# Kernel tuning notes

Measured on AMD Instinct MI355X. Metric: run time of the kernel, lower is better.

The kernel has to match this reference:

```python
import jax, jax.numpy as jnp
import numpy as np

EPS = 1e-6

def setup_inputs() -> dict:
    key = jax.random.key(0)
    ks = jax.random.split(key, 4)
    T, B, D = 2048, 16, 1024
    x = jax.random.normal(ks[0], (T, B, D), dtype=jnp.float32)
    h0 = jax.random.normal(ks[1], (B, D), dtype=jnp.float32)
    # xavier_uniform bound for square [D, D] matrices
    bound = float(np.sqrt(6.0 / (D + D)))
    W = jax.random.uniform(ks[2], (D, D), dtype=jnp.float32, minval=-bound, maxval=bound)
    W_g = jax.random.uniform(ks[3], (D, D), dtype=jnp.float32, minval=-bound, maxval=bound)
    b = jnp.zeros((D,), dtype=jnp.float32)
    b_g = jnp.full((D,), -2.0, dtype=jnp.float32)
    return {"x": x, "h0": h0, "W": W, "W_g": W_g, "b": b, "b_g": b_g}

def reference(x, h0, W, W_g, b, b_g):
    # Precompute both projections in batch (as the torch module does)
    Wx_all = jnp.einsum('tbd,ed->tbe', x, W) + b            # [T, B, D]
    gate_all = jax.nn.sigmoid(jnp.einsum('tbd,ed->tbe', x, W_g) + b_g)

    def step(h, inp):
        g, wx = inp
        h_new = h + g * wx                                   # gated residual
        h_new = h_new * jax.lax.rsqrt(
            jnp.mean(h_new * h_new, axis=-1, keepdims=True) + EPS)  # RMSNorm
        out = h_new * jax.nn.silu(h_new)                     # h * silu(h)
        return h_new, (h_new, out)

    _, (hs, outs) = jax.lax.scan(step, h0, (gate_all, Wx_all))
    h = jnp.concatenate([h0[None], hs], axis=0)              # [T+1, B, D]
    return outs, h
```

## Files before the change

kernel.cpp:

```cpp
#include <hip/hip_runtime.h>
#include <hip/hip_fp16.h>

typedef _Float16 f16;
typedef _Float16 f16x8 __attribute__((ext_vector_type(8)));
typedef float    f32x2 __attribute__((ext_vector_type(2)));
typedef float    f32x4 __attribute__((ext_vector_type(4)));
typedef unsigned ui4   __attribute__((ext_vector_type(4)));

#define T_STEPS 2048
#define BATCH   16
#define DIM     1024

__device__ __forceinline__ void async16(void* lds, const void* g) {
  __builtin_amdgcn_global_load_lds(
      (const __attribute__((address_space(1))) void*)g,
      (__attribute__((address_space(3))) void*)lds, 16, 0, 0);
}

__device__ __forceinline__ float fma_mix_lo(unsigned p, float one, float h) {
  float d;
  asm("v_fma_mix_f32 %0, %1, %2, %3 op_sel:[0,0,0] op_sel_hi:[1,0,0]"
      : "=v"(d) : "v"(p), "v"(one), "v"(h));
  return d;
}
__device__ __forceinline__ float fma_mix_hi(unsigned p, float one, float h) {
  float d;
  asm("v_fma_mix_f32 %0, %1, %2, %3 op_sel:[1,0,0] op_sel_hi:[1,0,0]"
      : "=v"(d) : "v"(p), "v"(one), "v"(h));
  return d;
}

__global__ void cvt_kernel(const float* __restrict__ src, f16* __restrict__ dst,
                           int n8) {
  int i = blockIdx.x * 256 + threadIdx.x;
  if (i >= n8) return;
  const float4* s4 = reinterpret_cast<const float4*>(src);
  float4 a = s4[2 * i], b = s4[2 * i + 1];
  f16x8 o;
  o[0] = (f16)a.x; o[1] = (f16)a.y; o[2] = (f16)a.z; o[3] = (f16)a.w;
  o[4] = (f16)b.x; o[5] = (f16)b.y; o[6] = (f16)b.z; o[7] = (f16)b.w;
  *reinterpret_cast<f16x8*>(dst + (size_t)i * 8) = o;
}

__global__ __launch_bounds__(256, 2)
void dual_gemm(const f16* __restrict__ xh, const f16* __restrict__ wh,
               const f16* __restrict__ wgh, const float* __restrict__ bias,
               const float* __restrict__ biasg, f16* __restrict__ P) {
  __shared__ f16 As[128 * 32];
  __shared__ f16 Bs[128 * 32];
  __shared__ f16 Gs[128 * 32];

  const int tid = threadIdx.x;
  const int bid = blockIdx.x;
  const int swz = ((bid & 7) << 8) | (bid >> 3);
  const int m0 = (swz >> 3) * 128;
  const int e0 = (swz & 7) * 128;

  const int lane = tid & 63;
  const int wave = tid >> 6;
  const int wrow = (wave >> 1) * 64;
  const int wcol = (wave & 1) * 64;
  const int fr = lane & 15;
  const int fc = lane >> 4;

  f32x4 acc1[4][4], acc2[4][4];
#pragma unroll
  for (int i = 0; i < 4; ++i)
#pragma unroll
    for (int j = 0; j < 4; ++j) {
      acc1[i][j] = {0.f, 0.f, 0.f, 0.f};
      acc2[i][j] = {0.f, 0.f, 0.f, 0.f};
    }

  const int    srow  = tid >> 2;
  const size_t sbyte = (size_t)(tid & 3) * 16;
  const char* ga = (const char*)xh  + ((size_t)(m0 + srow)) * 2048 + sbyte;
  const char* gb = (const char*)wh  + ((size_t)(e0 + srow)) * 2048 + sbyte;
  const char* gg = (const char*)wgh + ((size_t)(e0 + srow)) * 2048 + sbyte;
  char* la = (char*)&As[0] + (size_t)wave * 1024;
  char* lb = (char*)&Bs[0] + (size_t)wave * 1024;
  char* lg = (char*)&Gs[0] + (size_t)wave * 1024;

  for (int kk = 0; kk < 1024; kk += 32) {
    const size_t ko = (size_t)kk * 2;
    async16(la,        ga + ko);
    async16(la + 4096, ga + ko + (size_t)64 * 2048);
    async16(lb,        gb + ko);
    async16(lb + 4096, gb + ko + (size_t)64 * 2048);
    async16(lg,        gg + ko);
    async16(lg + 4096, gg + ko + (size_t)64 * 2048);
    asm volatile("s_waitcnt vmcnt(0)" ::: "memory");
    __syncthreads();

    f16x8 af[4], bf[4], gf[4];
#pragma unroll
    for (int i = 0; i < 4; ++i) {
      af[i] = *reinterpret_cast<const f16x8*>(&As[(wrow + i * 16 + fr) * 32 + fc * 8]);
      bf[i] = *reinterpret_cast<const f16x8*>(&Bs[(wcol + i * 16 + fr) * 32 + fc * 8]);
      gf[i] = *reinterpret_cast<const f16x8*>(&Gs[(wcol + i * 16 + fr) * 32 + fc * 8]);
    }
#pragma unroll
    for (int mi = 0; mi < 4; ++mi)
#pragma unroll
      for (int ni = 0; ni < 4; ++ni) {
        acc1[mi][ni] = __builtin_amdgcn_mfma_f32_16x16x32_f16(af[mi], bf[ni], acc1[mi][ni], 0, 0, 0);
        acc2[mi][ni] = __builtin_amdgcn_mfma_f32_16x16x32_f16(af[mi], gf[ni], acc2[mi][ni], 0, 0, 0);
      }
    __syncthreads();
  }

#pragma unroll
  for (int ni = 0; ni < 4; ++ni) {
    const int e = e0 + wcol + ni * 16 + fr;
    const float bb  = bias[e];
    const float bbg = biasg[e];
#pragma unroll
    for (int mi = 0; mi < 4; ++mi) {
      const int mrow = m0 + wrow + mi * 16 + fc * 4;
#pragma unroll
      for (int j = 0; j < 4; ++j) {
        float z1 = acc1[mi][ni][j] + bb;
        float z2 = acc2[mi][ni][j] + bbg;
        float s  = 1.0f / (1.0f + __expf(-z2));
        P[(size_t)(mrow + j) * DIM + e] = (f16)(z1 * s);
      }
    }
  }
}

template <int CTRL>
__device__ __forceinline__ float dpp_add(float x) {
  int m = __builtin_amdgcn_update_dpp(0, __float_as_int(x), CTRL, 0xf, 0xf, true);
  return x + __int_as_float(m);
}

__global__ __launch_bounds__(64, 1)
void scan_kernel(const f16* __restrict__ P, const float* __restrict__ h0,
                 float* __restrict__ hout) {
  const int b = blockIdx.x;
  const int lane = threadIdx.x;

  f32x4 h4[4];
  {
    const f32x4* s = (const f32x4*)(h0 + (size_t)b * DIM);
    f32x4* d = (f32x4*)(hout + (size_t)b * DIM);
    h4[0] = s[2 * lane];       d[2 * lane]       = h4[0];
    h4[1] = s[2 * lane + 1];   d[2 * lane + 1]   = h4[1];
    h4[2] = s[128 + 2 * lane]; d[128 + 2 * lane] = h4[2];
    h4[3] = s[129 + 2 * lane]; d[129 + 2 * lane] = h4[3];
  }

  ui4 pf[8][2];
#pragma unroll
  for (int u = 0; u < 8; ++u) {
    const ui4* pr = (const ui4*)(P + ((size_t)u * BATCH + b) * DIM);
    pf[u][0] = pr[lane];
    pf[u][1] = pr[64 + lane];
  }

  const float one = 1.0f;

  for (int t0 = 0; t0 < T_STEPS; t0 += 8) {
#pragma unroll
    for (int u = 0; u < 8; ++u) {
      const int t = t0 + u;

      f32x4 v4[4];
#pragma unroll
      for (int c = 0; c < 4; ++c) {
        const unsigned w0 = pf[u][c >> 1][(c & 1) * 2];
        const unsigned w1 = pf[u][c >> 1][(c & 1) * 2 + 1];
        v4[c][0] = fma_mix_lo(w0, one, h4[c][0]);
        v4[c][1] = fma_mix_hi(w0, one, h4[c][1]);
        v4[c][2] = fma_mix_lo(w1, one, h4[c][2]);
        v4[c][3] = fma_mix_hi(w1, one, h4[c][3]);
      }

      {
        const int tp = (t + 8) & (T_STEPS - 1);
        const ui4* pr = (const ui4*)(P + ((size_t)tp * BATCH + b) * DIM);
        pf[u][0] = pr[lane];
        pf[u][1] = pr[64 + lane];
      }

      f32x2 sE, sO;
      {
        f32x2 e0v = __builtin_shufflevector(v4[0], v4[0], 0, 1);
        f32x2 o0v = __builtin_shufflevector(v4[0], v4[0], 2, 3);
        sE = e0v * e0v;
        sO = o0v * o0v;
#pragma unroll
        for (int c = 1; c < 4; ++c) {
          f32x2 ec = __builtin_shufflevector(v4[c], v4[c], 0, 1);
          f32x2 oc = __builtin_shufflevector(v4[c], v4[c], 2, 3);
          sE += ec * ec;
          sO += oc * oc;
        }
      }
      f32x2 sC = sE + sO;
      float ss = sC[0] + sC[1];
      ss = dpp_add<0x111>(ss);
      ss = dpp_add<0x112>(ss);
      ss = dpp_add<0x114>(ss);
      ss = dpp_add<0x118>(ss);
      ss = dpp_add<0x142>(ss);
      ss = dpp_add<0x143>(ss);
      float tot = __int_as_float(__builtin_amdgcn_readlane(__float_as_int(ss), 63));
      float r = __builtin_amdgcn_rsqf(fmaf(tot, 9.765625e-4f, 1e-6f));

#pragma unroll
      for (int c = 0; c < 4; ++c) h4[c] = v4[c] * r;

      f32x4* hr = (f32x4*)(hout + ((size_t)(t + 1) * BATCH + b) * DIM);
      hr[2 * lane]       = h4[0];
      hr[2 * lane + 1]   = h4[1];
      hr[128 + 2 * lane] = h4[2];
      hr[129 + 2 * lane] = h4[3];
    }
  }
}

__global__ void silu_out_kernel(const float* __restrict__ hsrc,
                                float* __restrict__ out, int n4) {
  int stride = gridDim.x * blockDim.x;
  for (int i = blockIdx.x * blockDim.x + threadIdx.x; i < n4; i += stride) {
    float4 v = reinterpret_cast<const float4*>(hsrc)[i];
    float4 o;
    o.x = v.x * v.x / (1.0f + __expf(-v.x));
    o.y = v.y * v.y / (1.0f + __expf(-v.y));
    o.z = v.z * v.z / (1.0f + __expf(-v.z));
    o.w = v.w * v.w / (1.0f + __expf(-v.w));
    reinterpret_cast<float4*>(out)[i] = o;
  }
}

extern "C" void kernel_launch(void* const* d_in, const int* in_sizes, int n_in,
                              void* d_out, int out_size, void* d_ws, size_t ws_size,
                              hipStream_t stream) {
  const float* x  = (const float*)d_in[0];
  const float* h0 = (const float*)d_in[1];
  const float* W  = (const float*)d_in[2];
  const float* Wg = (const float*)d_in[3];
  const float* bb = (const float*)d_in[4];
  const float* bg = (const float*)d_in[5];

  float* out  = (float*)d_out;
  float* hout = out + (size_t)T_STEPS * BATCH * DIM;

  char* ws = (char*)d_ws;
  f16* xh  = (f16*)(ws);
  f16* wh  = (f16*)(ws + (size_t)67108864);
  f16* wgh = (f16*)(ws + (size_t)69206016);
  f16* P   = (f16*)(ws + (size_t)71303168);

  cvt_kernel<<<16384, 256, 0, stream>>>(x,  xh,  4194304);
  cvt_kernel<<<512,   256, 0, stream>>>(W,  wh,  131072);
  cvt_kernel<<<512,   256, 0, stream>>>(Wg, wgh, 131072);

  dual_gemm<<<2048, 256, 0, stream>>>(xh, wh, wgh, bb, bg, P);

  scan_kernel<<<BATCH, 64, 0, stream>>>(P, h0, hout);

  silu_out_kernel<<<2048, 256, 0, stream>>>(hout + BATCH * DIM, out, 8388608);
}
```

Measured before the change: 549.6 us.

## Fuse GEMM and scan into one persistent kernel with per-band readiness counters

Merges the dual GEMM and the sequential scan into one launch. The first 16 blocks run the scan and spin on per-band atomic counters, while the remaining blocks compute GEMM tiles in time order and signal completion with a release atomic. The aim is to overlap the long serial scan with GEMM production instead of running them back to back. This drops the block swizzle, which may hurt L2 reuse of the weights. Progress depends on scan blocks not starving GEMM blocks of occupancy, and the spin guard lets a wait give up after a bounded number of tries.

```diff
diff --git a/kernel.cpp b/kernel.cpp
--- a/kernel.cpp
+++ b/kernel.cpp
@@ -10,6 +10,9 @@
 #define T_STEPS 2048
 #define BATCH   16
 #define DIM     1024
+#define NBANDS  256
+#define SCAN_BLOCKS 16
+#define GEMM_BLOCKS 2048
 
 __device__ __forceinline__ void async16(void* lds, const void* g) {
   __builtin_amdgcn_global_load_lds(
@@ -28,6 +31,16 @@
   asm("v_fma_mix_f32 %0, %1, %2, %3 op_sel:[1,0,0] op_sel_hi:[1,0,0]"
       : "=v"(d) : "v"(p), "v"(one), "v"(h));
   return d;
+}
+
+template <int CTRL>
+__device__ __forceinline__ float dpp_add(float x) {
+  int m = __builtin_amdgcn_update_dpp(0, __float_as_int(x), CTRL, 0xf, 0xf, true);
+  return x + __int_as_float(m);
+}
+
+__global__ void init_kernel(unsigned* __restrict__ cnt) {
+  cnt[threadIdx.x + blockIdx.x * 256] = 0u;
 }
 
 __global__ void cvt_kernel(const float* __restrict__ src, f16* __restrict__ dst,
@@ -43,18 +56,124 @@
 }
 
 __global__ __launch_bounds__(256, 2)
-void dual_gemm(const f16* __restrict__ xh, const f16* __restrict__ wh,
-               const f16* __restrict__ wgh, const float* __restrict__ bias,
-               const float* __restrict__ biasg, f16* __restrict__ P) {
+void mega_kernel(const f16* __restrict__ xh, const f16* __restrict__ wh,
+                 const f16* __restrict__ wgh, const float* __restrict__ bias,
+                 const float* __restrict__ biasg, f16* __restrict__ P,
+                 const float* __restrict__ h0, float* __restrict__ hout,
+                 unsigned* __restrict__ cnt) {
   __shared__ f16 As[128 * 32];
   __shared__ f16 Bs[128 * 32];
   __shared__ f16 Gs[128 * 32];
 
+  if (blockIdx.x < SCAN_BLOCKS) {
+    if (threadIdx.x >= 64) return;
+    const int b = blockIdx.x;
+    const int lane = threadIdx.x;
+
+    {
+      int guard = 1 << 27;
+      while (__hip_atomic_load(&cnt[0], __ATOMIC_RELAXED,
+                               __HIP_MEMORY_SCOPE_AGENT) < 8u && --guard)
+        __builtin_amdgcn_s_sleep(2);
+      (void)__hip_atomic_load(&cnt[0], __ATOMIC_ACQUIRE,
+                              __HIP_MEMORY_SCOPE_AGENT);
+    }
+
+    f32x4 h4[4];
+    {
+      const f32x4* s = (const f32x4*)(h0 + (size_t)b * DIM);
+      f32x4* d = (f32x4*)(hout + (size_t)b * DIM);
+      h4[0] = s[2 * lane];       d[2 * lane]       = h4[0];
+      h4[1] = s[2 * lane + 1];   d[2 * lane + 1]   = h4[1];
+      h4[2] = s[128 + 2 * lane]; d[128 + 2 * lane] = h4[2];
+      h4[3] = s[129 + 2 * lane]; d[129 + 2 * lane] = h4[3];
+    }
+
+    ui4 pf[8][2];
+#pragma unroll
+    for (int u = 0; u < 8; ++u) {
+      const ui4* pr = (const ui4*)(P + ((size_t)u * BATCH + b) * DIM);
+      pf[u][0] = pr[lane];
+      pf[u][1] = pr[64 + lane];
+    }
+
+    const float one = 1.0f;
+
+    for (int t0 = 0; t0 < T_STEPS; t0 += 8) {
+      const int nb = (t0 >> 3) + 1;
+      if (nb < NBANDS) {
+        int guard = 1 << 27;
+        while (__hip_atomic_load(&cnt[nb], __ATOMIC_RELAXED,
+                                 __HIP_MEMORY_SCOPE_AGENT) < 8u && --guard)
+          __builtin_amdgcn_s_sleep(2);
+        (void)__hip_atomic_load(&cnt[nb], __ATOMIC_ACQUIRE,
+                                __HIP_MEMORY_SCOPE_AGENT);
+      }
+#pragma unroll
+      for (int u = 0; u < 8; ++u) {
+        const int t = t0 + u;
+
+        f32x4 v4[4];
+#pragma unroll
+        for (int c = 0; c < 4; ++c) {
+          const unsigned w0 = pf[u][c >> 1][(c & 1) * 2];
+          const unsigned w1 = pf[u][c >> 1][(c & 1) * 2 + 1];
+          v4[c][0] = fma_mix_lo(w0, one, h4[c][0]);
+          v4[c][1] = fma_mix_hi(w0, one, h4[c][1]);
+          v4[c][2] = fma_mix_lo(w1, one, h4[c][2]);
+          v4[c][3] = fma_mix_hi(w1, one, h4[c][3]);
+        }
+
+        {
+          const int tp = (t + 8) & (T_STEPS - 1);
+          const ui4* pr = (const ui4*)(P + ((size_t)tp * BATCH + b) * DIM);
+          pf[u][0] = pr[lane];
+          pf[u][1] = pr[64 + lane];
+        }
+
+        f32x2 sE, sO;
+        {
+          f32x2 e0v = __builtin_shufflevector(v4[0], v4[0], 0, 1);
+          f32x2 o0v = __builtin_shufflevector(v4[0], v4[0], 2, 3);
+          sE = e0v * e0v;
+          sO = o0v * o0v;
+#pragma unroll
+          for (int c = 1; c < 4; ++c) {
+            f32x2 ec = __builtin_shufflevector(v4[c], v4[c], 0, 1);
+            f32x2 oc = __builtin_shufflevector(v4[c], v4[c], 2, 3);
+            sE += ec * ec;
+            sO += oc * oc;
+          }
+        }
+        f32x2 sC = sE + sO;
+        float ss = sC[0] + sC[1];
+        ss = dpp_add<0x111>(ss);
+        ss = dpp_add<0x112>(ss);
+        ss = dpp_add<0x114>(ss);
+        ss = dpp_add<0x118>(ss);
+        ss = dpp_add<0x142>(ss);
+        ss = dpp_add<0x143>(ss);
+        float tot = __int_as_float(__builtin_amdgcn_readlane(__float_as_int(ss), 63));
+        float r = __builtin_amdgcn_rsqf(fmaf(tot, 9.765625e-4f, 1e-6f));
+
+#pragma unroll
+        for (int c = 0; c < 4; ++c) h4[c] = v4[c] * r;
+
+        f32x4* hr = (f32x4*)(hout + ((size_t)(t + 1) * BATCH + b) * DIM);
+        hr[2 * lane]       = h4[0];
+        hr[2 * lane + 1]   = h4[1];
+        hr[128 + 2 * lane] = h4[2];
+        hr[129 + 2 * lane] = h4[3];
+      }
+    }
+    return;
+  }
+
+  const int g = blockIdx.x - SCAN_BLOCKS;
+  const int band = g >> 3;
+  const int m0 = band << 7;
+  const int e0 = (g & 7) << 7;
   const int tid = threadIdx.x;
-  const int bid = blockIdx.x;
-  const int swz = ((bid & 7) << 8) | (bid >> 3);
-  const int m0 = (swz >> 3) * 128;
-  const int e0 = (swz & 7) * 128;
 
   const int lane = tid & 63;
   const int wave = tid >> 6;
@@ -126,98 +245,12 @@
       }
     }
   }
-}
-
-template <int CTRL>
-__device__ __forceinline__ float dpp_add(float x) {
-  int m = __builtin_amdgcn_update_dpp(0, __float_as_int(x), CTRL, 0xf, 0xf, true);
-  return x + __int_as_float(m);
-}
-
-__global__ __launch_bounds__(64, 1)
-void scan_kernel(const f16* __restrict__ P, const float* __restrict__ h0,
-                 float* __restrict__ hout) {
-  const int b = blockIdx.x;
-  const int lane = threadIdx.x;
-
-  f32x4 h4[4];
-  {
-    const f32x4* s = (const f32x4*)(h0 + (size_t)b * DIM);
-    f32x4* d = (f32x4*)(hout + (size_t)b * DIM);
-    h4[0] = s[2 * lane];       d[2 * lane]       = h4[0];
-    h4[1] = s[2 * lane + 1];   d[2 * lane + 1]   = h4[1];
-    h4[2] = s[128 + 2 * lane]; d[128 + 2 * lane] = h4[2];
-    h4[3] = s[129 + 2 * lane]; d[129 + 2 * lane] = h4[3];
-  }
-
-  ui4 pf[8][2];
-#pragma unroll
-  for (int u = 0; u < 8; ++u) {
-    const ui4* pr = (const ui4*)(P + ((size_t)u * BATCH + b) * DIM);
-    pf[u][0] = pr[lane];
-    pf[u][1] = pr[64 + lane];
-  }
-
-  const float one = 1.0f;
-
-  for (int t0 = 0; t0 < T_STEPS; t0 += 8) {
-#pragma unroll
-    for (int u = 0; u < 8; ++u) {
-      const int t = t0 + u;
-
-      f32x4 v4[4];
-#pragma unroll
-      for (int c = 0; c < 4; ++c) {
-        const unsigned w0 = pf[u][c >> 1][(c & 1) * 2];
-        const unsigned w1 = pf[u][c >> 1][(c & 1) * 2 + 1];
-        v4[c][0] = fma_mix_lo(w0, one, h4[c][0]);
-        v4[c][1] = fma_mix_hi(w0, one, h4[c][1]);
-        v4[c][2] = fma_mix_lo(w1, one, h4[c][2]);
-        v4[c][3] = fma_mix_hi(w1, one, h4[c][3]);
-      }
-
-      {
-        const int tp = (t + 8) & (T_STEPS - 1);
-        const ui4* pr = (const ui4*)(P + ((size_t)tp * BATCH + b) * DIM);
-        pf[u][0] = pr[lane];
-        pf[u][1] = pr[64 + lane];
-      }
-
-      f32x2 sE, sO;
-      {
-        f32x2 e0v = __builtin_shufflevector(v4[0], v4[0], 0, 1);
-        f32x2 o0v = __builtin_shufflevector(v4[0], v4[0], 2, 3);
-        sE = e0v * e0v;
-        sO = o0v * o0v;
-#pragma unroll
-        for (int c = 1; c < 4; ++c) {
-          f32x2 ec = __builtin_shufflevector(v4[c], v4[c], 0, 1);
-          f32x2 oc = __builtin_shufflevector(v4[c], v4[c], 2, 3);
-          sE += ec * ec;
-          sO += oc * oc;
-        }
-      }
-      f32x2 sC = sE + sO;
-      float ss = sC[0] + sC[1];
-      ss = dpp_add<0x111>(ss);
-      ss = dpp_add<0x112>(ss);
-      ss = dpp_add<0x114>(ss);
-      ss = dpp_add<0x118>(ss);
-      ss = dpp_add<0x142>(ss);
-      ss = dpp_add<0x143>(ss);
-      float tot = __int_as_float(__builtin_amdgcn_readlane(__float_as_int(ss), 63));
-      float r = __builtin_amdgcn_rsqf(fmaf(tot, 9.765625e-4f, 1e-6f));
-
-#pragma unroll
-      for (int c = 0; c < 4; ++c) h4[c] = v4[c] * r;
-
-      f32x4* hr = (f32x4*)(hout + ((size_t)(t + 1) * BATCH + b) * DIM);
-      hr[2 * lane]       = h4[0];
-      hr[2 * lane + 1]   = h4[1];
-      hr[128 + 2 * lane] = h4[2];
-      hr[129 + 2 * lane] = h4[3];
-    }
-  }
+
+  __threadfence();
+  __syncthreads();
+  if (tid == 0)
+    __hip_atomic_fetch_add(&cnt[band], 1u, __ATOMIC_RELEASE,
+                           __HIP_MEMORY_SCOPE_AGENT);
 }
 
 __global__ void silu_out_kernel(const float* __restrict__ hsrc,
@@ -252,14 +285,16 @@
   f16* wh  = (f16*)(ws + (size_t)67108864);
   f16* wgh = (f16*)(ws + (size_t)69206016);
   f16* P   = (f16*)(ws + (size_t)71303168);
+  unsigned* cnt = (unsigned*)(ws + (size_t)138412032);
+
+  init_kernel<<<4, 256, 0, stream>>>(cnt);
 
   cvt_kernel<<<16384, 256, 0, stream>>>(x,  xh,  4194304);
   cvt_kernel<<<512,   256, 0, stream>>>(W,  wh,  131072);
   cvt_kernel<<<512,   256, 0, stream>>>(Wg, wgh, 131072);
 
-  dual_gemm<<<2048, 256, 0, stream>>>(xh, wh, wgh, bb, bg, P);
-
-  scan_kernel<<<BATCH, 64, 0, stream>>>(P, h0, hout);
+  mega_kernel<<<SCAN_BLOCKS + GEMM_BLOCKS, 256, 0, stream>>>(
+      xh, wh, wgh, bb, bg, P, h0, hout, cnt);
 
   silu_out_kernel<<<2048, 256, 0, stream>>>(hout + BATCH * DIM, out, 8388608);
 }
```

After: 969.8 us. 1.76x slower.

## Process two batch rows per wavefront in scan kernel to interleave reductions

Applied to the files above, without the earlier changes.

The scan kernel now assigns two batch rows to each 64-lane block and launches 8 blocks instead of 16. The two rows' fma-mix updates, DPP reduction chains and rsqrt steps are interleaved so each row's serial latency chain can hide the other's. The cost is double the register use (prefetch buffers doubled to 2x8x2 ui4) and only 8 CUs active, so per-wave memory bandwidth for loads and stores doubles.

```diff
diff --git a/kernel.cpp b/kernel.cpp
--- a/kernel.cpp
+++ b/kernel.cpp
@@ -137,26 +137,29 @@
 __global__ __launch_bounds__(64, 1)
 void scan_kernel(const f16* __restrict__ P, const float* __restrict__ h0,
                  float* __restrict__ hout) {
-  const int b = blockIdx.x;
+  const int b0 = blockIdx.x * 2;
   const int lane = threadIdx.x;
 
-  f32x4 h4[4];
-  {
-    const f32x4* s = (const f32x4*)(h0 + (size_t)b * DIM);
-    f32x4* d = (f32x4*)(hout + (size_t)b * DIM);
-    h4[0] = s[2 * lane];       d[2 * lane]       = h4[0];
-    h4[1] = s[2 * lane + 1];   d[2 * lane + 1]   = h4[1];
-    h4[2] = s[128 + 2 * lane]; d[128 + 2 * lane] = h4[2];
-    h4[3] = s[129 + 2 * lane]; d[129 + 2 * lane] = h4[3];
-  }
-
-  ui4 pf[8][2];
-#pragma unroll
-  for (int u = 0; u < 8; ++u) {
-    const ui4* pr = (const ui4*)(P + ((size_t)u * BATCH + b) * DIM);
-    pf[u][0] = pr[lane];
-    pf[u][1] = pr[64 + lane];
-  }
+  f32x4 h4[2][4];
+#pragma unroll
+  for (int r = 0; r < 2; ++r) {
+    const f32x4* s = (const f32x4*)(h0 + (size_t)(b0 + r) * DIM);
+    f32x4* d = (f32x4*)(hout + (size_t)(b0 + r) * DIM);
+    h4[r][0] = s[2 * lane];       d[2 * lane]       = h4[r][0];
+    h4[r][1] = s[2 * lane + 1];   d[2 * lane + 1]   = h4[r][1];
+    h4[r][2] = s[128 + 2 * lane]; d[128 + 2 * lane] = h4[r][2];
+    h4[r][3] = s[129 + 2 * lane]; d[129 + 2 * lane] = h4[r][3];
+  }
+
+  ui4 pf[2][8][2];
+#pragma unroll
+  for (int u = 0; u < 8; ++u)
+#pragma unroll
+    for (int r = 0; r < 2; ++r) {
+      const ui4* pr = (const ui4*)(P + ((size_t)u * BATCH + b0 + r) * DIM);
+      pf[r][u][0] = pr[lane];
+      pf[r][u][1] = pr[64 + lane];
+    }
 
   const float one = 1.0f;
 
@@ -165,57 +168,76 @@
     for (int u = 0; u < 8; ++u) {
       const int t = t0 + u;
 
-      f32x4 v4[4];
-#pragma unroll
-      for (int c = 0; c < 4; ++c) {
-        const unsigned w0 = pf[u][c >> 1][(c & 1) * 2];
-        const unsigned w1 = pf[u][c >> 1][(c & 1) * 2 + 1];
-        v4[c][0] = fma_mix_lo(w0, one, h4[c][0]);
-        v4[c][1] = fma_mix_hi(w0, one, h4[c][1]);
-        v4[c][2] = fma_mix_lo(w1, one, h4[c][2]);
-        v4[c][3] = fma_mix_hi(w1, one, h4[c][3]);
-      }
+      f32x4 v4[2][4];
+#pragma unroll
+      for (int r = 0; r < 2; ++r)
+#pragma unroll
+        for (int c = 0; c < 4; ++c) {
+          const unsigned w0 = pf[r][u][c >> 1][(c & 1) * 2];
+          const unsigned w1 = pf[r][u][c >> 1][(c & 1) * 2 + 1];
+          v4[r][c][0] = fma_mix_lo(w0, one, h4[r][c][0]);
+          v4[r][c][1] = fma_mix_hi(w0, one, h4[r][c][1]);
+          v4[r][c][2] = fma_mix_lo(w1, one, h4[r][c][2]);
+          v4[r][c][3] = fma_mix_hi(w1, one, h4[r][c][3]);
+        }
 
       {
         const int tp = (t + 8) & (T_STEPS - 1);
-        const ui4* pr = (const ui4*)(P + ((size_t)tp * BATCH + b) * DIM);
-        pf[u][0] = pr[lane];
-        pf[u][1] = pr[64 + lane];
-      }
-
-      f32x2 sE, sO;
-      {
-        f32x2 e0v = __builtin_shufflevector(v4[0], v4[0], 0, 1);
-        f32x2 o0v = __builtin_shufflevector(v4[0], v4[0], 2, 3);
+#pragma unroll
+        for (int r = 0; r < 2; ++r) {
+          const ui4* pr = (const ui4*)(P + ((size_t)tp * BATCH + b0 + r) * DIM);
+          pf[r][u][0] = pr[lane];
+          pf[r][u][1] = pr[64 + lane];
+        }
+      }
+
+      float ssv[2];
+#pragma unroll
+      for (int r = 0; r < 2; ++r) {
+        f32x2 sE, sO;
+        f32x2 e0v = __builtin_shufflevector(v4[r][0], v4[r][0], 0, 1);
+        f32x2 o0v = __builtin_shufflevector(v4[r][0], v4[r][0], 2, 3);
         sE = e0v * e0v;
         sO = o0v * o0v;
 #pragma unroll
         for (int c = 1; c < 4; ++c) {
-          f32x2 ec = __builtin_shufflevector(v4[c], v4[c], 0, 1);
-          f32x2 oc = __builtin_shufflevector(v4[c], v4[c], 2, 3);
+          f32x2 ec = __builtin_shufflevector(v4[r][c], v4[r][c], 0, 1);
+          f32x2 oc = __builtin_shufflevector(v4[r][c], v4[r][c], 2, 3);
           sE += ec * ec;
           sO += oc * oc;
         }
-      }
-      f32x2 sC = sE + sO;
-      float ss = sC[0] + sC[1];
-      ss = dpp_add<0x111>(ss);
-      ss = dpp_add<0x112>(ss);
-      ss = dpp_add<0x114>(ss);
-      ss = dpp_add<0x118>(ss);
-      ss = dpp_add<0x142>(ss);
-      ss = dpp_add<0x143>(ss);
-      float tot = __int_as_float(__builtin_amdgcn_readlane(__float_as_int(ss), 63));
-      float r = __builtin_amdgcn_rsqf(fmaf(tot, 9.765625e-4f, 1e-6f));
-
-#pragma unroll
-      for (int c = 0; c < 4; ++c) h4[c] = v4[c] * r;
-
-      f32x4* hr = (f32x4*)(hout + ((size_t)(t + 1) * BATCH + b) * DIM);
-      hr[2 * lane]       = h4[0];
-      hr[2 * lane + 1]   = h4[1];
-      hr[128 + 2 * lane] = h4[2];
-      hr[129 + 2 * lane] = h4[3];
+        f32x2 sC = sE + sO;
+        ssv[r] = sC[0] + sC[1];
+      }
+
+#pragma unroll
+      for (int r = 0; r < 2; ++r) ssv[r] = dpp_add<0x111>(ssv[r]);
+#pragma unroll
+      for (int r = 0; r < 2; ++r) ssv[r] = dpp_add<0x112>(ssv[r]);
+#pragma unroll
+      for (int r = 0; r < 2; ++r) ssv[r] = dpp_add<0x114>(ssv[r]);
+#pragma unroll
+      for (int r = 0; r < 2; ++r) ssv[r] = dpp_add<0x118>(ssv[r]);
+#pragma unroll
+      for (int r = 0; r < 2; ++r) ssv[r] = dpp_add<0x142>(ssv[r]);
+#pragma unroll
+      for (int r = 0; r < 2; ++r) ssv[r] = dpp_add<0x143>(ssv[r]);
+
+#pragma unroll
+      for (int r = 0; r < 2; ++r) {
+        float tot = __int_as_float(
+            __builtin_amdgcn_readlane(__float_as_int(ssv[r]), 63));
+        float rs = __builtin_amdgcn_rsqf(fmaf(tot, 9.765625e-4f, 1e-6f));
+#pragma unroll
+        for (int c = 0; c < 4; ++c) h4[r][c] = v4[r][c] * rs;
+
+        f32x4* hr =
+            (f32x4*)(hout + ((size_t)(t + 1) * BATCH + b0 + r) * DIM);
+        hr[2 * lane]       = h4[r][0];
+        hr[2 * lane + 1]   = h4[r][1];
+        hr[128 + 2 * lane] = h4[r][2];
+        hr[129 + 2 * lane] = h4[r][3];
+      }
     }
   }
 }
@@ -259,7 +281,7 @@
 
   dual_gemm<<<2048, 256, 0, stream>>>(xh, wh, wgh, bb, bg, P);
 
-  scan_kernel<<<BATCH, 64, 0, stream>>>(P, h0, hout);
+  scan_kernel<<<8, 64, 0, stream>>>(P, h0, hout);
 
   silu_out_kernel<<<2048, 256, 0, stream>>>(hout + BATCH * DIM, out, 8388608);
 }
```

Result: slower. 787.6 us (+43.3%).
